# Performance work log

Measured on AMD Instinct MI355X. Metric: run time of the kernel, lower is better.

Reference implementation:

```python
import jax, jax.numpy as jnp
import numpy as np

EMBED_DIM = 512
N_QUERY = 4096
N_PROTO = 1024


def setup_inputs() -> dict:
    key = jax.random.key(0)
    k_q, k_p, k_wmu = jax.random.split(key, 3)
    d = EMBED_DIM
    bound = (6.0 / (d + d)) ** 0.5
    return {
        "query_features": jax.random.normal(k_q, (N_QUERY, d), dtype=jnp.float32),
        "prototypes": jax.random.normal(k_p, (N_PROTO, d), dtype=jnp.float32),
        "weight_mu": jax.random.uniform(k_wmu, (d, d), dtype=jnp.float32, minval=-bound, maxval=bound),
        "weight_rho": jnp.full((d, d), -3.0, dtype=jnp.float32),
        "bias_mu": jnp.zeros((d,), dtype=jnp.float32),
        "bias_rho": jnp.full((d,), 0.01, dtype=jnp.float32),
        "n_samples": 10,
    }


def reference(query_features, prototypes, weight_mu, weight_rho, bias_mu, bias_rho, n_samples):
    d = weight_mu.shape[0]
    # softplus reparameterization (same each iteration in the original loop)
    weight_sigma = jnp.log1p(jnp.exp(weight_rho))  # [d, d]
    bias_sigma = jnp.log1p(jnp.exp(bias_rho))      # [d]
    # batched MC weight/bias samples: [S, d, d] and [S, d]
    key = jax.random.key(42)
    kw, kb = jax.random.split(key)
    eps_w = jax.random.normal(kw, (n_samples, d, d), dtype=weight_mu.dtype)
    eps_b = jax.random.normal(kb, (n_samples, d), dtype=bias_mu.dtype)
    w = weight_mu[None] + weight_sigma[None] * eps_w   # [S, d, d]
    b = bias_mu[None] + bias_sigma[None] * eps_b       # [S, d]
    # F.linear(x, W_sample.T, b) == x @ W_sample + b
    tq = jnp.einsum('qd,sde->sqe', query_features, w) + b[:, None, :]  # [S, Q, d]
    # cdist via ||a||^2 + ||b||^2 - 2 a.b
    sq_q = jnp.sum(tq * tq, axis=-1)                    # [S, Q]
    sq_p = jnp.sum(prototypes * prototypes, axis=-1)    # [P]
    cross = jnp.einsum('sqe,pe->sqp', tq, prototypes)   # [S, Q, P]
    sqd = sq_q[:, :, None] + sq_p[None, None, :] - 2.0 * cross
    dists = jnp.sqrt(jnp.maximum(sqd, 1e-12))           # [S, Q, P]
    mean_distance = jnp.mean(dists, axis=0)
    uncertainty = jnp.std(dists, axis=0, ddof=1)        # torch.std is unbiased
    return mean_distance, uncertainty
```

## Files before the change

kernel.cpp:

```cpp
#include <hip/hip_runtime.h>
#include <stdint.h>

#define NS 10
#define DIM 512
#define NQ 4096
#define NP 1024

typedef unsigned short ushort_t;
typedef __bf16 bf16el_t;
typedef bf16el_t bf16x8 __attribute__((ext_vector_type(8)));
typedef float floatx4 __attribute__((ext_vector_type(4)));

__host__ __device__ __forceinline__ uint32_t rotl32(uint32_t x, int r) {
  return (x << r) | (x >> (32 - r));
}

__host__ __device__ __forceinline__ void threefry2x32(uint32_t k0, uint32_t k1,
                                                      uint32_t x0, uint32_t x1,
                                                      uint32_t* o0, uint32_t* o1) {
  uint32_t ks2 = k0 ^ k1 ^ 0x1BD11BDAu;
  x0 += k0; x1 += k1;
#define TF_R(r) { x0 += x1; x1 = rotl32(x1, r); x1 ^= x0; }
  TF_R(13) TF_R(15) TF_R(26) TF_R(6)   x0 += k1;  x1 += ks2 + 1u;
  TF_R(17) TF_R(29) TF_R(16) TF_R(24)  x0 += ks2; x1 += k0 + 2u;
  TF_R(13) TF_R(15) TF_R(26) TF_R(6)   x0 += k0;  x1 += k1 + 3u;
  TF_R(17) TF_R(29) TF_R(16) TF_R(24)  x0 += k1;  x1 += ks2 + 4u;
  TF_R(13) TF_R(15) TF_R(26) TF_R(6)   x0 += ks2; x1 += k0 + 5u;
#undef TF_R
  *o0 = x0; *o1 = x1;
}

__device__ __forceinline__ uint32_t jax_random_bits(uint32_t k0, uint32_t k1, uint32_t idx) {
  uint32_t o0, o1;
  threefry2x32(k0, k1, 0u, idx, &o0, &o1);
  return o0 ^ o1;
}

__device__ __forceinline__ float erfinvf_xla(float x) {
  float w = -log1pf(-x * x);
  float p;
  if (w < 5.0f) {
    w -= 2.5f;
    p = 2.81022636e-08f;
    p = fmaf(p, w, 3.43273939e-07f);
    p = fmaf(p, w, -3.5233877e-06f);
    p = fmaf(p, w, -4.39150654e-06f);
    p = fmaf(p, w, 0.00021858087f);
    p = fmaf(p, w, -0.00125372503f);
    p = fmaf(p, w, -0.00417768164f);
    p = fmaf(p, w, 0.246640727f);
    p = fmaf(p, w, 1.50140941f);
  } else {
    w = sqrtf(w) - 3.0f;
    p = -0.000200214257f;
    p = fmaf(p, w, 0.000100950558f);
    p = fmaf(p, w, 0.00134934322f);
    p = fmaf(p, w, -0.00367342844f);
    p = fmaf(p, w, 0.00573950773f);
    p = fmaf(p, w, -0.0076224613f);
    p = fmaf(p, w, 0.00943887047f);
    p = fmaf(p, w, 1.00167406f);
    p = fmaf(p, w, 2.83297682f);
  }
  return p * x;
}

__device__ __forceinline__ float jax_bits_to_normal(uint32_t bits) {
  float f = __uint_as_float((bits >> 9) | 0x3F800000u) - 1.0f;
  float u = f * 2.0f - 0.99999994f;
  u = fmaxf(u, -0.99999994f);
  return 1.41421356f * erfinvf_xla(u);
}

__device__ __forceinline__ float softplusf(float x) { return log1pf(expf(x)); }

__device__ __forceinline__ float bf2f(ushort_t u) {
  return __uint_as_float(((uint32_t)u) << 16);
}
__device__ __forceinline__ ushort_t f2bf(float f) {
  uint32_t u = __float_as_uint(f);
  u += 0x7FFFu + ((u >> 16) & 1u);
  return (ushort_t)(u >> 16);
}

__device__ __forceinline__ void gll16(const void* g, void* l) {
  __builtin_amdgcn_global_load_lds(
      (const __attribute__((address_space(1))) uint32_t*)g,
      (__attribute__((address_space(3))) uint32_t*)l, 16, 0, 0);
}

__global__ __launch_bounds__(256) void prep_kernel(const float* __restrict__ qf,
                                                   const float* __restrict__ pf,
                                                   const float* __restrict__ wmu,
                                                   const float* __restrict__ wrho,
                                                   const float* __restrict__ bmu,
                                                   const float* __restrict__ brho,
                                                   ushort_t* __restrict__ wt,
                                                   ushort_t* __restrict__ qb,
                                                   ushort_t* __restrict__ pb,
                                                   float* __restrict__ sqp,
                                                   float* __restrict__ bvec,
                                                   float* __restrict__ sqq,
                                                   uint32_t kw0, uint32_t kw1,
                                                   uint32_t kb0, uint32_t kb1) {
  __shared__ __align__(16) ushort_t lsW[64 * 64];
  const int blk = blockIdx.x;
  const int tid = threadIdx.x;
  if (blk < 640) {
    const int s = blk >> 6;
    const int rem = blk & 63;
    const int k0 = (rem >> 3) * 64;
    const int e0 = (rem & 7) * 64;
    const int r = tid >> 2;
    const int ch = tid & 3;
    const int kg = k0 + r;
    const int eg = e0 + ch * 16;
    const float* mup = wmu + kg * DIM + eg;
    const float* rhop = wrho + kg * DIM + eg;
    __align__(16) ushort_t wv[16];
#pragma unroll
    for (int v = 0; v < 4; ++v) {
      float4 m4 = *(const float4*)(mup + v * 4);
      float4 r4 = *(const float4*)(rhop + v * 4);
      float ms[4] = {m4.x, m4.y, m4.z, m4.w};
      float rs[4] = {r4.x, r4.y, r4.z, r4.w};
#pragma unroll
      for (int u = 0; u < 4; ++u) {
        uint32_t e = (uint32_t)(eg + v * 4 + u);
        uint32_t eps_idx = ((uint32_t)s << 18) | ((uint32_t)kg << 9) | e;
        float n = jax_bits_to_normal(jax_random_bits(kw0, kw1, eps_idx));
        wv[v * 4 + u] = f2bf(ms[u] + softplusf(rs[u]) * n);
      }
    }
    ushort_t* lrow = lsW + r * 64;
    *(uint4*)&lrow[((2 * ch) ^ (r & 7)) << 3]     = *(const uint4*)&wv[0];
    *(uint4*)&lrow[((2 * ch + 1) ^ (r & 7)) << 3] = *(const uint4*)&wv[8];
    __syncthreads();
    const int er = tid >> 2;
    const int kc = tid & 3;
    __align__(16) ushort_t ov[16];
#pragma unroll
    for (int j = 0; j < 16; ++j) {
      int k = kc * 16 + j;
      ov[j] = lsW[k * 64 + ((((er >> 3) ^ (k & 7)) << 3)) + (er & 7)];
    }
    ushort_t* orow = wt + (size_t)s * (DIM * DIM) + (size_t)(e0 + er) * DIM + k0 + kc * 16;
    *(uint4*)&orow[0] = *(const uint4*)&ov[0];
    *(uint4*)&orow[8] = *(const uint4*)&ov[8];
  } else if (blk < 2688) {
    int i = ((blk - 640) * 256 + tid) * 4;
    float4 v = *(const float4*)&qf[i];
    uint2 r;
    r.x = (uint32_t)f2bf(v.x) | ((uint32_t)f2bf(v.y) << 16);
    r.y = (uint32_t)f2bf(v.z) | ((uint32_t)f2bf(v.w) << 16);
    *(uint2*)&qb[i] = r;
  } else if (blk < 2944) {
    int p = (blk - 2688) * 4 + (tid >> 6);
    int lane = tid & 63;
    const float* src = pf + p * DIM + lane * 8;
    float4 a = *(const float4*)src;
    float4 b = *(const float4*)(src + 4);
    float vals[8] = {a.x, a.y, a.z, a.w, b.x, b.y, b.z, b.w};
    ushort_t o[8];
    float ss = 0.f;
#pragma unroll
    for (int i = 0; i < 8; ++i) {
      o[i] = f2bf(vals[i]);
      float f = bf2f(o[i]);
      ss += f * f;
    }
    *(uint4*)&pb[p * DIM + lane * 8] = *(const uint4*)o;
#pragma unroll
    for (int off = 32; off; off >>= 1) ss += __shfl_xor(ss, off, 64);
    if (lane == 0) sqp[p] = ss;
  } else if (blk < 2964) {
    uint32_t t2 = (blk - 2944) * 256u + tid;
    uint32_t e = t2 & 511u;
    uint32_t bits = jax_random_bits(kb0, kb1, t2);
    float n = jax_bits_to_normal(bits);
    bvec[t2] = bmu[e] + softplusf(brho[e]) * n;
  } else {
    int i = (blk - 2964) * 256 + tid;
    sqq[i] = 0.f;
  }
}

__global__ __launch_bounds__(256) void gemm_tq_kernel(const ushort_t* __restrict__ qb,
                                                      const ushort_t* __restrict__ wt,
                                                      const float* __restrict__ bvec,
                                                      ushort_t* __restrict__ tq,
                                                      float* __restrict__ sqq) {
  __shared__ __align__(16) ushort_t lsA[128 * 64];
  __shared__ __align__(16) ushort_t lsB[128 * 64];
  const int lane = threadIdx.x & 63;
  const int wave = threadIdx.x >> 6;
  const int wm = wave >> 1, wn = wave & 1;
  const int qBase = blockIdx.x * 128;
  const int eBase = blockIdx.y * 128;
  const int s = blockIdx.z;
  const ushort_t* wbase = wt + (size_t)s * (DIM * DIM);
  const int srow = lane >> 3;
  const int scol = ((lane & 7) ^ srow) * 16;
  const char* gA = (const char*)qb + (size_t)(qBase + wave * 32 + srow) * (DIM * 2) + scol;
  const char* gB = (const char*)wbase + (size_t)(eBase + wave * 32 + srow) * (DIM * 2) + scol;
  char* lA = (char*)&lsA[wave * 32 * 64];
  char* lB = (char*)&lsB[wave * 32 * 64];
  const int cn = lane & 15;
  const int cn7 = cn & 7;
  const int jc = lane >> 4;
  const floatx4 fzero = {0.f, 0.f, 0.f, 0.f};
  floatx4 acc[4][4];
#pragma unroll
  for (int ei = 0; ei < 4; ++ei)
#pragma unroll
    for (int qi = 0; qi < 4; ++qi) acc[ei][qi] = fzero;

  for (int kt = 0; kt < 8; ++kt) {
    __syncthreads();
#pragma unroll
    for (int j = 0; j < 4; ++j) {
      gll16(gA + (size_t)j * 8 * (DIM * 2), lA + j * 1024);
      gll16(gB + (size_t)j * 8 * (DIM * 2), lB + j * 1024);
    }
    gA += 128; gB += 128;
    __syncthreads();
#pragma unroll
    for (int c = 0; c < 8; c += 4) {
      const int po = ((c + jc) ^ cn7) << 3;
      bf16x8 aF[4], bF[4];
#pragma unroll
      for (int qi = 0; qi < 4; ++qi)
        aF[qi] = *(const bf16x8*)&lsA[(wm * 64 + qi * 16 + cn) * 64 + po];
#pragma unroll
      for (int ei = 0; ei < 4; ++ei)
        bF[ei] = *(const bf16x8*)&lsB[(wn * 64 + ei * 16 + cn) * 64 + po];
#pragma unroll
      for (int ei = 0; ei < 4; ++ei)
#pragma unroll
        for (int qi = 0; qi < 4; ++qi)
          acc[ei][qi] = __builtin_amdgcn_mfma_f32_16x16x32_bf16(bF[ei], aF[qi], acc[ei][qi], 0, 0, 0);
    }
  }

  const size_t tqs = (size_t)s * (NQ * DIM);
  const int eW = eBase + wn * 64;
  float4 bv4[4];
#pragma unroll
  for (int ei = 0; ei < 4; ++ei)
    bv4[ei] = *(const float4*)&bvec[s * DIM + eW + ei * 16 + jc * 4];
#pragma unroll
  for (int qi = 0; qi < 4; ++qi) {
    const int q = qBase + wm * 64 + qi * 16 + cn;
    ushort_t* rowp = tq + tqs + (size_t)q * DIM + eW + jc * 4;
    float ss = 0.f;
#pragma unroll
    for (int ei = 0; ei < 4; ++ei) {
      float vv[4] = {acc[ei][qi][0] + bv4[ei].x, acc[ei][qi][1] + bv4[ei].y,
                     acc[ei][qi][2] + bv4[ei].z, acc[ei][qi][3] + bv4[ei].w};
      ushort_t us[4];
#pragma unroll
      for (int j = 0; j < 4; ++j) {
        us[j] = f2bf(vv[j]);
        float rv = bf2f(us[j]);
        ss += rv * rv;
      }
      uint2 pk;
      pk.x = (uint32_t)us[0] | ((uint32_t)us[1] << 16);
      pk.y = (uint32_t)us[2] | ((uint32_t)us[3] << 16);
      *(uint2*)&rowp[ei * 16] = pk;
    }
    ss += __shfl_xor(ss, 16, 64);
    ss += __shfl_xor(ss, 32, 64);
    if (jc == 0) atomicAdd(&sqq[s * NQ + q], ss);
  }
}

__global__ __launch_bounds__(256, 2) void gemm_dist_kernel(const ushort_t* __restrict__ tq,
                                                           const ushort_t* __restrict__ pb,
                                                           const float* __restrict__ sqq,
                                                           const float* __restrict__ sqp,
                                                           float* __restrict__ out) {
  __shared__ __align__(16) ushort_t lsA[4 * 64 * 64];
  __shared__ __align__(16) ushort_t lsB[128 * 64];
  const int lane = threadIdx.x & 63;
  const int wave = threadIdx.x >> 6;
  const int wm = wave >> 1;
  const int wn = wave & 1;
  const int qBase = blockIdx.x * 64;
  const int pBase = blockIdx.y * 128;
  const int srow = lane >> 3;
  const int scol = ((lane & 7) ^ srow) * 16;
  const int cn = lane & 15;
  const int cn7 = cn & 7;
  const int jc = lane >> 4;
  const int rq = jc * 4;
  const floatx4 fzero = {0.f, 0.f, 0.f, 0.f};
  const char* gAb = (const char*)tq + (size_t)(qBase + wave * 16 + srow) * (DIM * 2) + scol;
  const char* gBb = (const char*)pb + (size_t)(pBase + wave * 32 + srow) * (DIM * 2) + scol;
  char* lAw = (char*)lsA + wave * 2048;
  char* lBw = (char*)lsB + wave * 4096;
  int po[2];
#pragma unroll
  for (int c = 0; c < 2; ++c) po[c] = ((c * 4 + jc) ^ cn7) << 3;

  float sum[2][4][4] = {};
  float ssq[2][4][4] = {};
  float sqp_v[4];
#pragma unroll
  for (int ni = 0; ni < 4; ++ni) sqp_v[ni] = sqp[pBase + wn * 64 + ni * 16 + cn];

  for (int grp = 0; grp < 3; ++grp) {
    const int sbase = grp * 4;
    const int gsz = (grp == 2) ? 2 : 4;
    floatx4 acc[4][2][4];
#pragma unroll
    for (int sp = 0; sp < 4; ++sp)
#pragma unroll
      for (int mi = 0; mi < 2; ++mi)
#pragma unroll
        for (int ni = 0; ni < 4; ++ni) acc[sp][mi][ni] = fzero;

    const char* gAg = gAb + (size_t)sbase * (NQ * DIM * 2);
    const char* gBk = gBb;
    for (int kt = 0; kt < 8; ++kt) {
      __syncthreads();
#pragma unroll
      for (int sp = 0; sp < 4; ++sp)
        if (sp < gsz) {
          const char* gs = gAg + (size_t)sp * (NQ * DIM * 2);
          char* ls = lAw + sp * 8192;
          gll16(gs, ls);
          gll16(gs + (size_t)8 * (DIM * 2), ls + 1024);
        }
#pragma unroll
      for (int j = 0; j < 4; ++j)
        gll16(gBk + (size_t)j * 8 * (DIM * 2), lBw + j * 1024);
      gAg += 128; gBk += 128;
      __syncthreads();
#pragma unroll
      for (int c = 0; c < 2; ++c) {
        bf16x8 bF[4];
#pragma unroll
        for (int ni = 0; ni < 4; ++ni)
          bF[ni] = *(const bf16x8*)&lsB[(wn * 64 + ni * 16 + cn) * 64 + po[c]];
#pragma unroll
        for (int sp = 0; sp < 4; ++sp)
          if (sp < gsz) {
            bf16x8 aF[2];
#pragma unroll
            for (int mi = 0; mi < 2; ++mi)
              aF[mi] = *(const bf16x8*)&lsA[sp * 4096 + (wm * 32 + mi * 16 + cn) * 64 + po[c]];
#pragma unroll
            for (int mi = 0; mi < 2; ++mi)
#pragma unroll
              for (int ni = 0; ni < 4; ++ni)
                acc[sp][mi][ni] =
                    __builtin_amdgcn_mfma_f32_16x16x32_bf16(aF[mi], bF[ni], acc[sp][mi][ni], 0, 0, 0);
          }
      }
    }
#pragma unroll
    for (int sp = 0; sp < 4; ++sp)
      if (sp < gsz) {
        const int s = sbase + sp;
#pragma unroll
        for (int mi = 0; mi < 2; ++mi) {
          float4 aqv = *(const float4*)&sqq[s * NQ + qBase + wm * 32 + mi * 16 + rq];
          float aqa[4] = {aqv.x, aqv.y, aqv.z, aqv.w};
#pragma unroll
          for (int r = 0; r < 4; ++r) {
            float aq = aqa[r];
#pragma unroll
            for (int ni = 0; ni < 4; ++ni) {
              float sqd = fmaxf(fmaf(-2.0f, acc[sp][mi][ni][r], aq + sqp_v[ni]), 1e-12f);
              sum[mi][ni][r] += sqrtf(sqd);
              ssq[mi][ni][r] += sqd;
            }
          }
        }
      }
  }
#pragma unroll
  for (int mi = 0; mi < 2; ++mi)
#pragma unroll
    for (int ni = 0; ni < 4; ++ni)
#pragma unroll
      for (int r = 0; r < 4; ++r) {
        int q = qBase + wm * 32 + mi * 16 + rq + r;
        int p = pBase + wn * 64 + ni * 16 + cn;
        float sm = sum[mi][ni][r];
        float mean = sm * 0.1f;
        float var = (ssq[mi][ni][r] - sm * sm * 0.1f) * (1.0f / 9.0f);
        out[(size_t)q * NP + p] = mean;
        out[(size_t)NQ * NP + (size_t)q * NP + p] = sqrtf(fmaxf(var, 0.0f));
      }
}

extern "C" void kernel_launch(void* const* d_in, const int* in_sizes, int n_in,
                              void* d_out, int out_size, void* d_ws, size_t ws_size,
                              hipStream_t stream) {
  const float* qf   = (const float*)d_in[0];
  const float* pf   = (const float*)d_in[1];
  const float* wmu  = (const float*)d_in[2];
  const float* wrho = (const float*)d_in[3];
  const float* bmu  = (const float*)d_in[4];
  const float* brho = (const float*)d_in[5];
  float* out = (float*)d_out;
  char* ws = (char*)d_ws;
  ushort_t* wt   = (ushort_t*)(ws);
  ushort_t* qb   = (ushort_t*)(ws + 5242880);
  ushort_t* pb   = (ushort_t*)(ws + 9437184);
  float*    bvec = (float*)   (ws + 10485760);
  float*    sqp  = (float*)   (ws + 10506240);
  ushort_t* tq   = (ushort_t*)(ws + 10510336);
  float*    sqq  = (float*)   (ws + 52453376);

  uint32_t kw0, kw1, kb0, kb1;
  threefry2x32(0u, 42u, 0u, 0u, &kw0, &kw1);
  threefry2x32(0u, 42u, 0u, 1u, &kb0, &kb1);

  hipLaunchKernelGGL(prep_kernel, dim3(3124), dim3(256), 0, stream,
                     qf, pf, wmu, wrho, bmu, brho, wt, qb, pb, sqp, bvec, sqq,
                     kw0, kw1, kb0, kb1);
  hipLaunchKernelGGL(gemm_tq_kernel, dim3(32, 4, 10), dim3(256), 0, stream, qb, wt, bvec, tq, sqq);
  hipLaunchKernelGGL(gemm_dist_kernel, dim3(64, 8), dim3(256), 0, stream, tq, pb, sqq, sqp, out);
}
```

Measured before the change: 200.5 us.

## Load A operand fragments directly from global into registers, group samples by two

After: 243.1 us. 1.21x slower.

```diff
diff --git a/kernel.cpp b/kernel.cpp
--- a/kernel.cpp
+++ b/kernel.cpp
@@ -280,7 +280,6 @@
                                                            const float* __restrict__ sqq,
                                                            const float* __restrict__ sqp,
                                                            float* __restrict__ out) {
-  __shared__ __align__(16) ushort_t lsA[4 * 64 * 64];
   __shared__ __align__(16) ushort_t lsB[128 * 64];
   const int lane = threadIdx.x & 63;
   const int wave = threadIdx.x >> 6;
@@ -295,10 +294,12 @@
   const int jc = lane >> 4;
   const int rq = jc * 4;
   const floatx4 fzero = {0.f, 0.f, 0.f, 0.f};
-  const char* gAb = (const char*)tq + (size_t)(qBase + wave * 16 + srow) * (DIM * 2) + scol;
   const char* gBb = (const char*)pb + (size_t)(pBase + wave * 32 + srow) * (DIM * 2) + scol;
-  char* lAw = (char*)lsA + wave * 2048;
   char* lBw = (char*)lsB + wave * 4096;
+  const ushort_t* aBase[2];
+#pragma unroll
+  for (int mi = 0; mi < 2; ++mi)
+    aBase[mi] = tq + (size_t)(qBase + wm * 32 + mi * 16 + cn) * DIM + jc * 8;
   int po[2];
 #pragma unroll
   for (int c = 0; c < 2; ++c) po[c] = ((c * 4 + jc) ^ cn7) << 3;
@@ -309,33 +310,32 @@
 #pragma unroll
   for (int ni = 0; ni < 4; ++ni) sqp_v[ni] = sqp[pBase + wn * 64 + ni * 16 + cn];
 
-  for (int grp = 0; grp < 3; ++grp) {
-    const int sbase = grp * 4;
-    const int gsz = (grp == 2) ? 2 : 4;
-    floatx4 acc[4][2][4];
-#pragma unroll
-    for (int sp = 0; sp < 4; ++sp)
+  for (int grp = 0; grp < 5; ++grp) {
+    const int s0 = grp * 2;
+    floatx4 acc[2][2][4];
+#pragma unroll
+    for (int sp = 0; sp < 2; ++sp)
 #pragma unroll
       for (int mi = 0; mi < 2; ++mi)
 #pragma unroll
         for (int ni = 0; ni < 4; ++ni) acc[sp][mi][ni] = fzero;
 
-    const char* gAg = gAb + (size_t)sbase * (NQ * DIM * 2);
     const char* gBk = gBb;
     for (int kt = 0; kt < 8; ++kt) {
       __syncthreads();
 #pragma unroll
-      for (int sp = 0; sp < 4; ++sp)
-        if (sp < gsz) {
-          const char* gs = gAg + (size_t)sp * (NQ * DIM * 2);
-          char* ls = lAw + sp * 8192;
-          gll16(gs, ls);
-          gll16(gs + (size_t)8 * (DIM * 2), ls + 1024);
-        }
-#pragma unroll
       for (int j = 0; j < 4; ++j)
         gll16(gBk + (size_t)j * 8 * (DIM * 2), lBw + j * 1024);
-      gAg += 128; gBk += 128;
+      gBk += 128;
+      bf16x8 aR[2][2][2];
+#pragma unroll
+      for (int sp = 0; sp < 2; ++sp)
+#pragma unroll
+        for (int mi = 0; mi < 2; ++mi)
+#pragma unroll
+          for (int c = 0; c < 2; ++c)
+            aR[sp][mi][c] = *(const bf16x8*)&aBase[mi][(size_t)(s0 + sp) * (NQ * DIM) +
+                                                       kt * 64 + c * 32];
       __syncthreads();
 #pragma unroll
       for (int c = 0; c < 2; ++c) {
@@ -344,41 +344,34 @@
         for (int ni = 0; ni < 4; ++ni)
           bF[ni] = *(const bf16x8*)&lsB[(wn * 64 + ni * 16 + cn) * 64 + po[c]];
 #pragma unroll
-        for (int sp = 0; sp < 4; ++sp)
-          if (sp < gsz) {
-            bf16x8 aF[2];
-#pragma unroll
-            for (int mi = 0; mi < 2; ++mi)
-              aF[mi] = *(const bf16x8*)&lsA[sp * 4096 + (wm * 32 + mi * 16 + cn) * 64 + po[c]];
-#pragma unroll
-            for (int mi = 0; mi < 2; ++mi)
-#pragma unroll
-              for (int ni = 0; ni < 4; ++ni)
-                acc[sp][mi][ni] =
-                    __builtin_amdgcn_mfma_f32_16x16x32_bf16(aF[mi], bF[ni], acc[sp][mi][ni], 0, 0, 0);
-          }
+        for (int sp = 0; sp < 2; ++sp)
+#pragma unroll
+          for (int mi = 0; mi < 2; ++mi)
+#pragma unroll
+            for (int ni = 0; ni < 4; ++ni)
+              acc[sp][mi][ni] = __builtin_amdgcn_mfma_f32_16x16x32_bf16(
+                  aR[sp][mi][c], bF[ni], acc[sp][mi][ni], 0, 0, 0);
       }
     }
 #pragma unroll
-    for (int sp = 0; sp < 4; ++sp)
-      if (sp < gsz) {
-        const int s = sbase + sp;
-#pragma unroll
-        for (int mi = 0; mi < 2; ++mi) {
-          float4 aqv = *(const float4*)&sqq[s * NQ + qBase + wm * 32 + mi * 16 + rq];
-          float aqa[4] = {aqv.x, aqv.y, aqv.z, aqv.w};
-#pragma unroll
-          for (int r = 0; r < 4; ++r) {
-            float aq = aqa[r];
-#pragma unroll
-            for (int ni = 0; ni < 4; ++ni) {
-              float sqd = fmaxf(fmaf(-2.0f, acc[sp][mi][ni][r], aq + sqp_v[ni]), 1e-12f);
-              sum[mi][ni][r] += sqrtf(sqd);
-              ssq[mi][ni][r] += sqd;
-            }
+    for (int sp = 0; sp < 2; ++sp) {
+      const int s = s0 + sp;
+#pragma unroll
+      for (int mi = 0; mi < 2; ++mi) {
+        float4 aqv = *(const float4*)&sqq[s * NQ + qBase + wm * 32 + mi * 16 + rq];
+        float aqa[4] = {aqv.x, aqv.y, aqv.z, aqv.w};
+#pragma unroll
+        for (int r = 0; r < 4; ++r) {
+          float aq = aqa[r];
+#pragma unroll
+          for (int ni = 0; ni < 4; ++ni) {
+            float sqd = fmaxf(fmaf(-2.0f, acc[sp][mi][ni][r], aq + sqp_v[ni]), 1e-12f);
+            sum[mi][ni][r] += sqrtf(sqd);
+            ssq[mi][ni][r] += sqd;
           }
         }
       }
+    }
   }
 #pragma unroll
   for (int mi = 0; mi < 2; ++mi)
```
